# Kernel optimization log

Measured on AMD Instinct MI355X. Metric: run time of the kernel, lower is better.

The kernel has to match this reference:

```python
import jax, jax.numpy as jnp
import numpy as np

PATCH = 16; EMBED = 768; HEADS = 12; DHEAD = 64
DEPTH_PRE = 2; DEPTH_SHORT = 8; PRIOR = 0.2
SCALE = 1.0 / float(DHEAD) ** 0.5
LN_EPS = 1e-5


def _ln(x, g, b):
    m = jnp.mean(x, -1, keepdims=True)
    v = jnp.mean(jnp.square(x - m), -1, keepdims=True)
    return (x - m) * jax.lax.rsqrt(v + LN_EPS) * g + b


def _pos_emb(T, d):
    # pos_seq = T-1 .. 0 (descending), sinusoidal [T, d]
    pos = jnp.arange(T - 1, -1, -1, dtype=jnp.float32)
    inv_freq = 1.0 / (10000.0 ** (jnp.arange(0.0, d, 2.0, dtype=jnp.float32) / d))
    s = pos[:, None] * inv_freq[None, :]
    return jnp.concatenate([jnp.sin(s), jnp.cos(s)], axis=-1)


def _rel_shift(x):
    # Transformer-XL relative shift: pad one zero col, reshape, drop first row
    b, h, q, r = x.shape
    xp = jnp.pad(x, ((0, 0), (0, 0), (0, 0), (1, 0)))
    return xp.reshape(b, h, r + 1, q)[:, :, 1:, :].reshape(b, h, q, r)


def _layer(x, r_emb, rwb, rrb, qkv_w, qkv_b, rn_w, rn_b, o_w, o_b,
           l1g, l1b, f1w, f1b, f2w, f2b, l2g, l2b):
    T, B, D = x.shape
    heads = x @ qkv_w.T + qkv_b
    q, k, v = jnp.split(heads, 3, axis=-1)
    q = q.reshape(T, B, HEADS, DHEAD)
    k = k.reshape(T, B, HEADS, DHEAD)
    v = v.reshape(T, B, HEADS, DHEAD)
    rk = (r_emb @ rn_w.T + rn_b).reshape(T, HEADS, DHEAD)
    AC = jnp.einsum('ibnd,jbnd->bnij', q + rwb, k)
    BD = _rel_shift(jnp.einsum('ibnd,jnd->bnij', q + rrb, rk))
    prob = jax.nn.softmax(SCALE * (AC + BD), axis=-1)  # no attn_mask in this model
    av = jnp.einsum('bnij,jbnd->ibnd', prob, v).reshape(T, B, D)
    x = _ln(x + av @ o_w.T + o_b, l1g, l1b)  # post-lnorm
    h = jax.nn.gelu(x @ f1w.T + f1b, approximate=False)
    return _ln(x + h @ f2w.T + f2b, l2g, l2b)


def setup_inputs() -> dict:
    key = jax.random.key(0)
    ks = jax.random.split(key, 16)
    f = jnp.float32
    D, H, FF, L = EMBED, HEADS, 3072, DEPTH_PRE + DEPTH_SHORT

    def w(k, shape, s=0.02):
        return jax.random.normal(k, shape, dtype=f) * s

    return {
        'x': jax.random.normal(ks[0], (32, 3, 224, 224), dtype=f),
        'patch_w': w(ks[1], (D, 3, PATCH, PATCH)),
        'patch_b': jnp.zeros((D,), f),
        'r_w_bias': jnp.zeros((H, DHEAD), f),
        'r_r_bias': jnp.zeros((H, DHEAD), f),
        'qkv_w': w(ks[2], (L, 3 * D, D)),
        'qkv_b': jnp.zeros((L, 3 * D), f),
        'rnet_w': w(ks[3], (L, D, D)),
        'rnet_b': jnp.zeros((L, D), f),
        'onet_w': w(ks[4], (L, D, D)),
        'onet_b': jnp.zeros((L, D), f),
        'ln1_g': jnp.ones((L, D), f), 'ln1_b': jnp.zeros((L, D), f),
        'ff1_w': w(ks[5], (L, FF, D)),
        'ff1_b': jnp.zeros((L, FF), f),
        'ff2_w': w(ks[6], (L, D, FF)),
        'ff2_b': jnp.zeros((L, D), f),
        'ln2_g': jnp.ones((L, D), f), 'ln2_b': jnp.zeros((L, D), f),
        'null_tok': w(ks[7], (1, 1, D)),
        'down_g': jnp.ones((D,), f), 'down_b': jnp.zeros((D,), f),
        'head_w': w(ks[8], (1000, D)),
        'head_b': jnp.zeros((1000,), f),
    }


def reference(x, patch_w, patch_b, r_w_bias, r_r_bias, qkv_w, qkv_b,
              rnet_w, rnet_b, onet_w, onet_b, ln1_g, ln1_b,
              ff1_w, ff1_b, ff2_w, ff2_b, ln2_g, ln2_b,
              null_tok, down_g, down_b, head_w, head_b):
    B = x.shape[0]
    # patch embed: conv stride=kernel=PATCH, NCHW
    h = jax.lax.conv_general_dilated(
        x, patch_w, (PATCH, PATCH), 'VALID',
        dimension_numbers=('NCHW', 'OIHW', 'NCHW')) + patch_b[None, :, None, None]
    T = h.shape[2] * h.shape[3]  # 196
    h = h.reshape(B, EMBED, T).transpose(2, 0, 1)  # [T, B, D]
    r = _pos_emb(T, EMBED)

    def blk(z, i, rr):
        return _layer(z, rr, r_w_bias, r_r_bias,
                      qkv_w[i], qkv_b[i], rnet_w[i], rnet_b[i],
                      onet_w[i], onet_b[i], ln1_g[i], ln1_b[i],
                      ff1_w[i], ff1_b[i], ff2_w[i], ff2_b[i],
                      ln2_g[i], ln2_b[i])

    for i in range(DEPTH_PRE):
        h = blk(h, i, r)

    # flop_measure boundaries: 1 every interval tokens; downsample = segment mean
    interval = max(1, int(1 / PRIOR))  # 5
    bnd = (jnp.arange(T) % interval == 0).astype(h.dtype)
    seg = (jnp.cumsum(bnd) - bnd).astype(jnp.int32)  # segment id per token
    S = int(np.ceil(T / interval))  # 40 (static)
    onehot = jax.nn.one_hot(seg, S, dtype=h.dtype)  # [T, S]
    pool = onehot / jnp.sum(onehot, axis=0, keepdims=True)
    short = jnp.einsum('tbd,ts->sbd', h, pool)  # [S, B, D]
    short = jnp.concatenate(
        [jnp.broadcast_to(null_tok.reshape(1, 1, EMBED), (1, B, EMBED)), short], axis=0)
    h = _ln(short, down_g, down_b)  # [S+1, B, D]

    r2 = _pos_emb(h.shape[0], EMBED)
    for i in range(DEPTH_PRE, DEPTH_PRE + DEPTH_SHORT):
        h = blk(h, i, r2)

    return h.mean(axis=0) @ head_w.T + head_b  # [B, 1000]
```

## Files before the change

kernel.cpp:

```cpp
#include <hip/hip_runtime.h>
#include <hip/hip_bf16.h>
#include <math.h>
#include <stdint.h>

typedef __bf16 bf16;
typedef __bf16 bf16x8 __attribute__((ext_vector_type(8)));
typedef float  f32x4  __attribute__((ext_vector_type(4)));

#define NB   32
#define ED   768
#define NH   12
#define DHD  64
#define FFD  3072
#define TT1  196
#define TT2  41
#define TPM  208
#define MM1  6272
#define MM2  1408
#define M2R  1312
#define BHN  384
#define LTOT 10
#define SCL  0.125f

__device__ __forceinline__ void gload_lds16(const bf16* g, bf16* l) {
  __builtin_amdgcn_global_load_lds(
      (__attribute__((address_space(1))) void*)(uintptr_t)g,
      (__attribute__((address_space(3))) void*)(uint32_t)(uintptr_t)l,
      16, 0, 0);
}

__device__ __forceinline__ float block_sum(float v, float* red, int tid) {
#pragma unroll
  for (int o = 32; o; o >>= 1) v += __shfl_xor(v, o);
  if ((tid & 63) == 0) red[tid >> 6] = v;
  __syncthreads();
  float t = red[0] + red[1] + red[2] + red[3];
  __syncthreads();
  return t;
}

__device__ __forceinline__ float gelu_f(float v) {
  const float u = v * (0.7978845608f + 0.0356774081f * v * v);
  const float t = 1.0f - 2.0f / (__expf(2.0f * u) + 1.0f);
  return 0.5f * v * (1.0f + t);
}

__device__ __forceinline__ bf16x8 cvt8(const float* __restrict__ s) {
  const f32x4 a = *(const f32x4*)s;
  const f32x4 b = *(const f32x4*)(s + 4);
  bf16x8 o;
#pragma unroll
  for (int j = 0; j < 4; ++j) { o[j] = (bf16)a[j]; o[4 + j] = (bf16)b[j]; }
  return o;
}

__global__ void k_cvt(const float* __restrict__ s, bf16* __restrict__ d, long n8) {
  for (long i = (long)blockIdx.x * 256 + threadIdx.x; i < n8; i += (long)gridDim.x * 256)
    *(bf16x8*)&d[i * 8] = cvt8(&s[i * 8]);
}

__global__ void k_cvt4(const float* __restrict__ a, const float* __restrict__ b,
                       const float* __restrict__ c, const float* __restrict__ d,
                       bf16* __restrict__ oa, bf16* __restrict__ ob,
                       bf16* __restrict__ oc, bf16* __restrict__ od,
                       int na8, int nb8, int nc8, int nd8) {
  const long tot = (long)na8 + nb8 + nc8 + nd8;
  for (long i = (long)blockIdx.x * 256 + threadIdx.x; i < tot; i += (long)gridDim.x * 256) {
    if (i < na8) *(bf16x8*)&oa[i * 8] = cvt8(&a[i * 8]);
    else if (i < (long)na8 + nb8) { const long j = i - na8; *(bf16x8*)&ob[j * 8] = cvt8(&b[j * 8]); }
    else if (i < (long)na8 + nb8 + nc8) { const long j = i - na8 - nb8; *(bf16x8*)&oc[j * 8] = cvt8(&c[j * 8]); }
    else { const long j = i - na8 - nb8 - nc8; *(bf16x8*)&od[j * 8] = cvt8(&d[j * 8]); }
  }
}

__global__ void k_posemb(bf16* __restrict__ out, int T) {
  const int t = blockIdx.x, c = threadIdx.x;
  float v = 0.0f;
  if (t < T) {
    const float pos = (float)(T - 1 - t);
    const int ci = (c < 384) ? c : c - 384;
    const float invf = expf(-(float)ci * (9.210340371976184f / 384.0f));
    const float a = pos * invf;
    v = (c < 384) ? sinf(a) : cosf(a);
  }
  out[(long)t * ED + c] = (bf16)v;
}

__global__ void k_im2col(const float* __restrict__ x, bf16* __restrict__ A0) {
  const long idx = (long)blockIdx.x * 256 + threadIdx.x;
  if (idx >= (long)MM1 * ED) return;
  const int row = (int)(idx / ED), k = (int)(idx % ED);
  const int t = row >> 5, b = row & 31;
  const int c = k >> 8, rem = k & 255, i = rem >> 4, j = rem & 15;
  const int py = t / 14, px = t % 14;
  A0[idx] = (bf16)x[((long)(b * 3 + c) * 224 + (py * 16 + i)) * 224 + px * 16 + j];
}

template <int EPI>
__global__ __launch_bounds__(256) void k_gemm(const bf16* __restrict__ A, const bf16* __restrict__ Bw,
                                              const float* __restrict__ bias,
                                              float* __restrict__ Cf, bf16* __restrict__ Cb,
                                              int M, int N, int K, int LDK) {
  __shared__ __align__(16) bf16 As[3][128 * 32];
  __shared__ __align__(16) bf16 Bs[3][128 * 32];
  const int tid = threadIdx.x;
  const int l = tid & 63, w = tid >> 6;
  const int wr = w >> 1, wc = w & 1;
  const int m0 = blockIdx.y * 128, n0 = blockIdx.x * 128;
  const long koff = (long)blockIdx.z * K;
  const int srow = l >> 2;
  const int scol = ((l & 3) ^ ((l >> 3) & 3)) * 8;
  f32x4 acc[4][4] = {};
  const int nt = K >> 5;

  auto stage = [&](int t, int b) {
    const int kt = t << 5;
#pragma unroll
    for (int p = 0; p < 2; ++p) {
      const int rbase = w * 32 + p * 16;
      gload_lds16(&A[(long)(m0 + rbase + srow) * LDK + koff + kt + scol], &As[b][rbase * 32]);
      gload_lds16(&Bw[(long)(n0 + rbase + srow) * LDK + koff + kt + scol], &Bs[b][rbase * 32]);
    }
  };

  stage(0, 0);
  stage(1, 1);

  int cur = 0;
  for (int t = 0; t < nt; ++t) {
    if (t + 2 < nt) {
      stage(t + 2, cur == 0 ? 2 : cur - 1);
      asm volatile("s_waitcnt vmcnt(8)" ::: "memory");
    } else if (t + 1 < nt) {
      asm volatile("s_waitcnt vmcnt(4)" ::: "memory");
    } else {
      asm volatile("s_waitcnt vmcnt(0)" ::: "memory");
    }
    __builtin_amdgcn_s_barrier();
    {
      bf16x8 af[4], bg[4];
      const int ub = l >> 4;
#pragma unroll
      for (int m = 0; m < 4; ++m) {
        const int row = wr * 64 + m * 16 + (l & 15);
        af[m] = *(const bf16x8*)&As[cur][row * 32 + (ub ^ ((row >> 1) & 3)) * 8];
      }
#pragma unroll
      for (int n = 0; n < 4; ++n) {
        const int row = wc * 64 + n * 16 + (l & 15);
        bg[n] = *(const bf16x8*)&Bs[cur][row * 32 + (ub ^ ((row >> 1) & 3)) * 8];
      }
#pragma unroll
      for (int m = 0; m < 4; ++m)
#pragma unroll
        for (int n = 0; n < 4; ++n)
          acc[m][n] = __builtin_amdgcn_mfma_f32_16x16x32_bf16(af[m], bg[n], acc[m][n], 0, 0, 0);
    }
    asm volatile("s_waitcnt lgkmcnt(0)" ::: "memory");
    __builtin_amdgcn_s_barrier();
    cur = (cur == 2) ? 0 : cur + 1;
  }

  const long pbase = (EPI == 4) ? (long)blockIdx.z * M * N : 0;
#pragma unroll
  for (int m = 0; m < 4; ++m) {
    const int row = m0 + wr * 64 + m * 16 + 4 * (l >> 4);
#pragma unroll
    for (int n = 0; n < 4; ++n) {
      const int col = n0 + wc * 64 + n * 16 + (l & 15);
      const float bv = (EPI == 4) ? 0.0f : bias[col];
#pragma unroll
      for (int r = 0; r < 4; ++r) {
        const float v = acc[m][n][r] + bv;
        const long off = (long)(row + r) * N + col;
        if (EPI == 0) {
          Cf[off] = v;
        } else if (EPI == 1) {
          Cb[off] = (bf16)gelu_f(v);
        } else if (EPI == 2) {
          Cf[off] = v;
          Cb[off] = (bf16)v;
        } else if (EPI == 3) {
          Cb[off] = (bf16)v;
        } else {
          Cf[pbase + off] = v;
        }
      }
    }
  }
}

__global__ __launch_bounds__(256) void k_redk_ln(const float* __restrict__ P, const float* __restrict__ bias,
                                                 const float* __restrict__ g, const float* __restrict__ bb,
                                                 const float* __restrict__ xin,
                                                 float* __restrict__ xo, bf16* __restrict__ xbo,
                                                 int KS, long MN, int Mreal) {
  const int row = blockIdx.x, tid = threadIdx.x;
  const long base = (long)row * ED;
  __shared__ float red[4];
  if (row >= Mreal) {
#pragma unroll
    for (int e = 0; e < 3; ++e) { xo[base + tid + e * 256] = 0.0f; xbo[base + tid + e * 256] = (bf16)0.0f; }
    return;
  }
  float v[3];
#pragma unroll
  for (int e = 0; e < 3; ++e) {
    const int c = tid + e * 256;
    float a = bias[c] + xin[base + c];
    for (int ks = 0; ks < KS; ++ks) a += P[(long)ks * MN + base + c];
    v[e] = a;
  }
  const float mean = block_sum(v[0] + v[1] + v[2], red, tid) * (1.0f / ED);
  float sq = 0.0f;
#pragma unroll
  for (int e = 0; e < 3; ++e) { const float dd = v[e] - mean; sq += dd * dd; }
  const float var = block_sum(sq, red, tid) * (1.0f / ED);
  const float rs = rsqrtf(var + 1e-5f);
#pragma unroll
  for (int e = 0; e < 3; ++e) {
    const int c = tid + e * 256;
    const float o = (v[e] - mean) * rs * g[c] + bb[c];
    xo[base + c] = o;
    xbo[base + c] = (bf16)o;
  }
}

__global__ __launch_bounds__(256) void k_attn_pre(
    const bf16* __restrict__ heads, const float* __restrict__ rwb, const float* __restrict__ rrb,
    const bf16* __restrict__ rkb_l, bf16* __restrict__ avb) {
  const int r0 = blockIdx.x * 64;
  const int bh = blockIdx.y;
  const int b = bh / NH, n = bh % NH;
  const int tid = threadIdx.x;
  const int l = tid & 63, w = tid >> 6;
  __shared__ float Sl[64 * 209];
  __shared__ __align__(16) bf16 probl[64 * 232];
  __shared__ __align__(16) bf16 vTl[64 * 232];
  __shared__ float red4[256];
  __shared__ float rstat[64];

  for (int task = tid; task < 224 * 8; task += 256) {
    const int j = task >> 3, c8 = (task & 7) * 8;
    if (j < TT1) {
      const bf16x8 vv = *(const bf16x8*)&heads[((long)(j * NB + b)) * (3 * ED) + 2 * ED + n * 64 + c8];
#pragma unroll
      for (int e = 0; e < 8; ++e) vTl[(c8 + e) * 232 + j] = vv[e];
    } else {
#pragma unroll
      for (int e = 0; e < 8; ++e) vTl[(c8 + e) * 232 + j] = (bf16)0.0f;
    }
  }

  for (int tt = w; tt < 52; tt += 4) {
    const int ti = tt / 13, tj = tt % 13;
    const int ar = r0 + ti * 16 + (l & 15);
    const int br = tj * 16 + (l & 15);
    f32x4 c = {};
#pragma unroll
    for (int kk = 0; kk < 64; kk += 32) {
      const int col = kk + 8 * (l >> 4);
      bf16x8 qa = {}, kb = {};
      if (ar < TT1) qa = *(const bf16x8*)&heads[((long)(ar * NB + b)) * (3 * ED) + n * 64 + col];
      if (br < TT1) kb = *(const bf16x8*)&heads[((long)(br * NB + b)) * (3 * ED) + ED + n * 64 + col];
      bf16x8 qq;
#pragma unroll
      for (int e = 0; e < 8; ++e) qq[e] = (bf16)((float)qa[e] + rwb[n * 64 + col + e]);
      c = __builtin_amdgcn_mfma_f32_16x16x32_bf16(qq, kb, c, 0, 0, 0);
    }
    const int scol = tj * 16 + (l & 15);
    const int srb = ti * 16 + 4 * (l >> 4);
#pragma unroll
    for (int r = 0; r < 4; ++r) Sl[(srb + r) * 209 + scol] = SCL * c[r];
  }
  __syncthreads();

  for (int tt = w; tt < 65; tt += 4) {
    const int ta = tt / 13, tb = tt % 13;
    const int ar = r0 + ta * 16 + (l & 15);
    const int br = tb * 16 + (l & 15);
    f32x4 c = {};
#pragma unroll
    for (int kk = 0; kk < 64; kk += 32) {
      const int col = kk + 8 * (l >> 4);
      bf16x8 qa = {};
      if (ar < TT1) qa = *(const bf16x8*)&heads[((long)(ar * NB + b)) * (3 * ED) + n * 64 + col];
      const bf16x8 rk = *(const bf16x8*)&rkb_l[((long)n * TPM + br) * 64 + col];
      bf16x8 qq;
#pragma unroll
      for (int e = 0; e < 8; ++e) qq[e] = (bf16)((float)qa[e] + rrb[n * 64 + col + e]);
      c = __builtin_amdgcn_mfma_f32_16x16x32_bf16(qq, rk, c, 0, 0, 0);
    }
    const int bcol = tb * 16 + (l & 15);
    const int ab = r0 + ta * 16 + 4 * (l >> 4);
#pragma unroll
    for (int r = 0; r < 4; ++r) {
      const int a = ab + r;
      if (a < TT1 && bcol < TT1) {
        const int m = a * (TT1 + 1) + bcol + 1;
        if (m >= TT1) {
          const int i = m / TT1 - 1;
          const int j = m - (i + 1) * TT1;
          const int li = i - r0;
          if (li >= 0 && li < 64) Sl[li * 209 + j] += SCL * c[r];
        }
      }
    }
  }
  __syncthreads();

  const int sr = tid & 63, sg = tid >> 6;
  const bool rowok = (r0 + sr) < TT1;
  float pm = -3.0e38f;
  if (rowok) {
    const int j0 = sg * 49;
    for (int j = j0; j < j0 + 49; ++j) pm = fmaxf(pm, Sl[sr * 209 + j]);
  }
  red4[sr * 4 + sg] = pm;
  __syncthreads();
  if (sg == 0)
    rstat[sr] = fmaxf(fmaxf(red4[sr * 4], red4[sr * 4 + 1]), fmaxf(red4[sr * 4 + 2], red4[sr * 4 + 3]));
  __syncthreads();
  const float rm = rstat[sr];
  float ps = 0.0f;
  if (rowok) {
    const int j0 = sg * 49;
    for (int j = j0; j < j0 + 49; ++j) {
      const float e = __expf(Sl[sr * 209 + j] - rm);
      Sl[sr * 209 + j] = e;
      ps += e;
    }
  }
  red4[sr * 4 + sg] = ps;
  __syncthreads();
  if (sg == 0) {
    const float s = red4[sr * 4] + red4[sr * 4 + 1] + red4[sr * 4 + 2] + red4[sr * 4 + 3];
    rstat[sr] = (s > 0.0f) ? 1.0f / s : 0.0f;
  }
  __syncthreads();
  const float inv = rstat[sr];
  for (int j = sg * 56; j < sg * 56 + 56; ++j) {
    const float v = (rowok && j < TT1) ? Sl[sr * 209 + j] * inv : 0.0f;
    probl[sr * 232 + j] = (bf16)v;
  }
  __syncthreads();

  for (int tt = w; tt < 16; tt += 4) {
    const int ti = tt & 3, dj = tt >> 2;
    f32x4 c = {};
#pragma unroll
    for (int kk = 0; kk < 224; kk += 32) {
      const bf16x8 pa = *(const bf16x8*)&probl[(ti * 16 + (l & 15)) * 232 + kk + 8 * (l >> 4)];
      const bf16x8 vb = *(const bf16x8*)&vTl[(dj * 16 + (l & 15)) * 232 + kk + 8 * (l >> 4)];
      c = __builtin_amdgcn_mfma_f32_16x16x32_bf16(pa, vb, c, 0, 0, 0);
    }
    const int d = dj * 16 + (l & 15);
    const int ib = ti * 16 + 4 * (l >> 4);
#pragma unroll
    for (int r = 0; r < 4; ++r) {
      const int gi = r0 + ib + r;
      if (gi < TT1) avb[((long)(gi * NB + b)) * ED + n * 64 + d] = (bf16)c[r];
    }
  }
}

__global__ __launch_bounds__(256) void k_attn_short(
    const bf16* __restrict__ heads, const float* __restrict__ rwb, const float* __restrict__ rrb,
    const bf16* __restrict__ rkb_l, bf16* __restrict__ avb) {
  const int bh = blockIdx.x;
  const int b = bh / NH, n = bh % NH;
  const int tid = threadIdx.x;
  const int l = tid & 63, w = tid >> 6;
  __shared__ float Sl[48 * 49];
  __shared__ __align__(16) bf16 probl[48 * 72];
  __shared__ __align__(16) bf16 vTl[64 * 72];

  for (int task = tid; task < 48 * 8; task += 256) {
    const int j = task >> 3, c8 = (task & 7) * 8;
    if (j < TT2) {
      const bf16x8 vv = *(const bf16x8*)&heads[((long)(j * NB + b)) * (3 * ED) + 2 * ED + n * 64 + c8];
#pragma unroll
      for (int e = 0; e < 8; ++e) vTl[(c8 + e) * 72 + j] = vv[e];
    } else {
#pragma unroll
      for (int e = 0; e < 8; ++e) vTl[(c8 + e) * 72 + j] = (bf16)0.0f;
    }
  }
  for (int idx = tid; idx < 64 * 16; idx += 256)
    vTl[(idx & 63) * 72 + 48 + (idx >> 6)] = (bf16)0.0f;

  for (int tt = w; tt < 9; tt += 4) {
    const int ti = tt / 3, tj = tt % 3;
    const int ar = ti * 16 + (l & 15);
    const int br = tj * 16 + (l & 15);
    f32x4 c = {};
#pragma unroll
    for (int kk = 0; kk < 64; kk += 32) {
      const int col = kk + 8 * (l >> 4);
      bf16x8 qa = {}, kb = {};
      if (ar < 44) qa = *(const bf16x8*)&heads[((long)(ar * NB + b)) * (3 * ED) + n * 64 + col];
      if (br < 44) kb = *(const bf16x8*)&heads[((long)(br * NB + b)) * (3 * ED) + ED + n * 64 + col];
      bf16x8 qq;
#pragma unroll
      for (int e = 0; e < 8; ++e) qq[e] = (bf16)((float)qa[e] + rwb[n * 64 + col + e]);
      c = __builtin_amdgcn_mfma_f32_16x16x32_bf16(qq, kb, c, 0, 0, 0);
    }
    const int scol = tj * 16 + (l & 15);
    const int srb = ti * 16 + 4 * (l >> 4);
#pragma unroll
    for (int r = 0; r < 4; ++r) Sl[(srb + r) * 49 + scol] = SCL * c[r];
  }
  __syncthreads();

  for (int tt = w; tt < 9; tt += 4) {
    const int ti = tt / 3, tj = tt % 3;
    const int ar = ti * 16 + (l & 15);
    const int br = tj * 16 + (l & 15);
    f32x4 c = {};
#pragma unroll
    for (int kk = 0; kk < 64; kk += 32) {
      const int col = kk + 8 * (l >> 4);
      bf16x8 qa = {};
      if (ar < 44) qa = *(const bf16x8*)&heads[((long)(ar * NB + b)) * (3 * ED) + n * 64 + col];
      const bf16x8 rk = *(const bf16x8*)&rkb_l[((long)n * TPM + br) * 64 + col];
      bf16x8 qq;
#pragma unroll
      for (int e = 0; e < 8; ++e) qq[e] = (bf16)((float)qa[e] + rrb[n * 64 + col + e]);
      c = __builtin_amdgcn_mfma_f32_16x16x32_bf16(qq, rk, c, 0, 0, 0);
    }
    const int bcol = tj * 16 + (l & 15);
    const int ab = ti * 16 + 4 * (l >> 4);
#pragma unroll
    for (int r = 0; r < 4; ++r) {
      const int a = ab + r;
      if (a < TT2 && bcol < TT2) {
        const int m = a * (TT2 + 1) + bcol + 1;
        if (m >= TT2) {
          const int i = m / TT2 - 1;
          const int j = m - (i + 1) * TT2;
          Sl[i * 49 + j] += SCL * c[r];
        }
      }
    }
  }
  __syncthreads();

  if (tid < 48) {
    const int i = tid;
    if (i < TT2) {
      float mx = -3.0e38f;
      for (int j = 0; j < TT2; ++j) mx = fmaxf(mx, Sl[i * 49 + j]);
      float sm = 0.0f;
      for (int j = 0; j < TT2; ++j) { const float e = expf(Sl[i * 49 + j] - mx); Sl[i * 49 + j] = e; sm += e; }
      const float inv = 1.0f / sm;
      for (int j = 0; j < TT2; ++j) probl[i * 72 + j] = (bf16)(Sl[i * 49 + j] * inv);
      for (int j = TT2; j < 64; ++j) probl[i * 72 + j] = (bf16)0.0f;
    } else {
      for (int j = 0; j < 64; ++j) probl[i * 72 + j] = (bf16)0.0f;
    }
  }
  __syncthreads();

  for (int tt = w; tt < 12; tt += 4) {
    const int ti = tt % 3, dj = tt / 3;
    f32x4 c = {};
#pragma unroll
    for (int kk = 0; kk < 64; kk += 32) {
      const bf16x8 pa = *(const bf16x8*)&probl[(ti * 16 + (l & 15)) * 72 + kk + 8 * (l >> 4)];
      const bf16x8 vb = *(const bf16x8*)&vTl[(dj * 16 + (l & 15)) * 72 + kk + 8 * (l >> 4)];
      c = __builtin_amdgcn_mfma_f32_16x16x32_bf16(pa, vb, c, 0, 0, 0);
    }
    const int d = dj * 16 + (l & 15);
    const int ib = ti * 16 + 4 * (l >> 4);
#pragma unroll
    for (int r = 0; r < 4; ++r) {
      const int i = ib + r;
      if (i < TT2) avb[((long)(i * NB + b)) * ED + n * 64 + d] = (bf16)c[r];
    }
  }
}

__global__ void k_rkrepack(const float* __restrict__ rkall, bf16* __restrict__ rkb,
                           int T, int Ncols, int l0) {
  const int i = blockIdx.x, z = blockIdx.y, d = threadIdx.x;
  const float v = (i < T) ? rkall[(long)i * Ncols + z * ED + d] : 0.0f;
  const int n = d >> 6, dh = d & 63;
  rkb[(((long)(l0 + z) * NH + n) * TPM + i) * 64 + dh] = (bf16)v;
}

__global__ __launch_bounds__(256) void k_ln(const float* __restrict__ xin, const float* __restrict__ add,
                                            const float* __restrict__ g, const float* __restrict__ bb,
                                            float* __restrict__ xo, bf16* __restrict__ xbo, int Mreal) {
  const int row = blockIdx.x, tid = threadIdx.x;
  const long base = (long)row * ED;
  __shared__ float red[4];
  if (row >= Mreal) {
#pragma unroll
    for (int e = 0; e < 3; ++e) { xo[base + tid + e * 256] = 0.0f; xbo[base + tid + e * 256] = (bf16)0.0f; }
    return;
  }
  float v[3];
#pragma unroll
  for (int e = 0; e < 3; ++e) v[e] = xin[base + tid + e * 256] + add[base + tid + e * 256];
  const float mean = block_sum(v[0] + v[1] + v[2], red, tid) * (1.0f / ED);
  float sq = 0.0f;
#pragma unroll
  for (int e = 0; e < 3; ++e) { const float dd = v[e] - mean; sq += dd * dd; }
  const float var = block_sum(sq, red, tid) * (1.0f / ED);
  const float rs = rsqrtf(var + 1e-5f);
#pragma unroll
  for (int e = 0; e < 3; ++e) {
    const int c = tid + e * 256;
    const float o = (v[e] - mean) * rs * g[c] + bb[c];
    xo[base + c] = o;
    xbo[base + c] = (bf16)o;
  }
}

__global__ __launch_bounds__(256) void k_down(const float* __restrict__ x, const float* __restrict__ nullt,
                                              const float* __restrict__ g, const float* __restrict__ bb,
                                              float* __restrict__ xo, bf16* __restrict__ xbo) {
  const int row = blockIdx.x, tid = threadIdx.x;
  const long base = (long)row * ED;
  __shared__ float red[4];
  if (row >= TT2 * NB) {
#pragma unroll
    for (int e = 0; e < 3; ++e) { xo[base + tid + e * 256] = 0.0f; xbo[base + tid + e * 256] = (bf16)0.0f; }
    return;
  }
  const int s = row >> 5, b = row & 31;
  float v[3];
  if (s == 0) {
#pragma unroll
    for (int e = 0; e < 3; ++e) v[e] = nullt[tid + e * 256];
  } else {
    const int seg = s - 1;
    const int t0 = (seg == 0) ? 0 : (5 * seg - 4);
    const int cnt = (seg == 0) ? 1 : 5;
#pragma unroll
    for (int e = 0; e < 3; ++e) {
      float a = 0.0f;
      for (int tt = 0; tt < cnt; ++tt) a += x[((long)((t0 + tt) * NB + b)) * ED + tid + e * 256];
      v[e] = a / (float)cnt;
    }
  }
  const float mean = block_sum(v[0] + v[1] + v[2], red, tid) * (1.0f / ED);
  float sq = 0.0f;
#pragma unroll
  for (int e = 0; e < 3; ++e) { const float dd = v[e] - mean; sq += dd * dd; }
  const float var = block_sum(sq, red, tid) * (1.0f / ED);
  const float rs = rsqrtf(var + 1e-5f);
#pragma unroll
  for (int e = 0; e < 3; ++e) {
    const int c = tid + e * 256;
    const float o = (v[e] - mean) * rs * g[c] + bb[c];
    xo[base + c] = o;
    xbo[base + c] = (bf16)o;
  }
}

__global__ __launch_bounds__(256) void k_mean(const float* __restrict__ x2, float* __restrict__ xm) {
  const int b = blockIdx.x, tid = threadIdx.x;
#pragma unroll
  for (int e = 0; e < 3; ++e) {
    const int c = tid + e * 256;
    float a = 0.0f;
    for (int s = 0; s < TT2; ++s) a += x2[((long)(s * NB + b)) * ED + c];
    xm[(long)b * ED + c] = a * (1.0f / TT2);
  }
}

__global__ __launch_bounds__(256) void k_head(const float* __restrict__ xm, const float* __restrict__ hw,
                                              const float* __restrict__ hbias, float* __restrict__ out) {
  const int gid = blockIdx.x * 4 + (threadIdx.x >> 6);
  const int l = threadIdx.x & 63;
  if (gid >= NB * 1000) return;
  const int b = gid / 1000, n = gid % 1000;
  const float* xr = xm + (long)b * ED;
  const float* wr = hw + (long)n * ED;
  float a = 0.0f;
#pragma unroll
  for (int e = 0; e < 12; ++e) a += xr[l + 64 * e] * wr[l + 64 * e];
#pragma unroll
  for (int o = 32; o; o >>= 1) a += __shfl_xor(a, o);
  if (l == 0) out[(long)b * 1000 + n] = a + hbias[n];
}

extern "C" void kernel_launch(void* const* d_in, const int* in_sizes, int n_in,
                              void* d_out, int out_size, void* d_ws, size_t ws_size,
                              hipStream_t stream) {
  const float* in_x     = (const float*)d_in[0];
  const float* patch_w  = (const float*)d_in[1];
  const float* patch_b  = (const float*)d_in[2];
  const float* r_w_bias = (const float*)d_in[3];
  const float* r_r_bias = (const float*)d_in[4];
  const float* qkv_w    = (const float*)d_in[5];
  const float* qkv_b    = (const float*)d_in[6];
  const float* rnet_w   = (const float*)d_in[7];
  const float* rnet_b   = (const float*)d_in[8];
  const float* onet_w   = (const float*)d_in[9];
  const float* onet_b   = (const float*)d_in[10];
  const float* ln1_g    = (const float*)d_in[11];
  const float* ln1_b    = (const float*)d_in[12];
  const float* ff1_w    = (const float*)d_in[13];
  const float* ff1_b    = (const float*)d_in[14];
  const float* ff2_w    = (const float*)d_in[15];
  const float* ff2_b    = (const float*)d_in[16];
  const float* ln2_g    = (const float*)d_in[17];
  const float* ln2_b    = (const float*)d_in[18];
  const float* null_tok = (const float*)d_in[19];
  const float* down_g   = (const float*)d_in[20];
  const float* down_b   = (const float*)d_in[21];
  const float* head_w   = (const float*)d_in[22];
  const float* head_b   = (const float*)d_in[23];
  float* out = (float*)d_out;

  char* base = (char*)d_ws;
  size_t off = 0;
  auto take = [&](size_t bytes) -> char* {
    char* r = base + off;
    off += (bytes + 255) & ~(size_t)255;
    return r;
  };

  float* x    = (float*)take((size_t)MM1 * ED * 4);
  bf16*  xb   = (bf16*)take((size_t)MM1 * ED * 2);
  float* x2   = (float*)take((size_t)MM2 * ED * 4);
  bf16*  xb2  = (bf16*)take((size_t)MM2 * ED * 2);
  bf16*  rkb  = (bf16*)take((size_t)LTOT * NH * TPM * 64 * 2);
  bf16*  rbf  = (bf16*)take((size_t)256 * ED * 2);
  bf16*  r2bf = (bf16*)take((size_t)128 * ED * 2);
  float* xm   = (float*)take((size_t)NB * ED * 4);

  char* arenaW = take((size_t)(2304 * 768 + 768 * 768 + 3072 * 768 + 768 * 3072) * 2);
  bf16* wq = (bf16*)arenaW;
  bf16* wo = wq + (size_t)2304 * 768;
  bf16* w1 = wo + (size_t)768 * 768;
  bf16* w2 = w1 + (size_t)3072 * 768;
  bf16* wrnet  = (bf16*)arenaW;
  bf16* wpatch = wrnet + (size_t)LTOT * 768 * 768;

  char* arenaQ = take((size_t)MM1 * ED * 2 + (size_t)4 * MM2 * ED * 4);
  bf16*  A0 = (bf16*)arenaQ;
  float* P  = (float*)arenaQ;

  char* arenaH = take((size_t)MM1 * 3 * ED * 2);
  bf16*  headsb = (bf16*)arenaH;
  float* rkall1 = (float*)arenaH;
  float* rkall2 = (float*)(arenaH + (size_t)256 * 1536 * 4);

  char* arenaS = take((size_t)MM1 * ED * 2 + (size_t)MM1 * ED * 4 + (size_t)MM1 * FFD * 2);
  bf16*  avb  = (bf16*)arenaS;
  float* gout = (float*)(arenaS + (size_t)MM1 * ED * 2);
  bf16*  hb   = (bf16*)(arenaS + (size_t)MM1 * ED * 2 + (size_t)MM1 * ED * 4);

  if (off > ws_size) return;

  k_posemb<<<dim3(256), dim3(768), 0, stream>>>(rbf, TT1);
  k_posemb<<<dim3(128), dim3(768), 0, stream>>>(r2bf, TT2);
  k_cvt<<<dim3(1024), dim3(256), 0, stream>>>(rnet_w, wrnet, (long)LTOT * 768 * 768 / 8);
  k_cvt<<<dim3(288), dim3(256), 0, stream>>>(patch_w, wpatch, (long)768 * 768 / 8);
  k_im2col<<<dim3((MM1 * ED + 255) / 256), dim3(256), 0, stream>>>(in_x, A0);
  k_gemm<2><<<dim3(6, 49, 1), dim3(256), 0, stream>>>(A0, wpatch, patch_b, x, xb, MM1, ED, ED, ED);
  k_gemm<0><<<dim3(12, 2, 1), dim3(256), 0, stream>>>(rbf, wrnet, rnet_b, rkall1, nullptr, 256, 1536, ED, ED);
  k_gemm<0><<<dim3(48, 1, 1), dim3(256), 0, stream>>>(r2bf, wrnet + (size_t)2 * 768 * 768, rnet_b + 2 * 768,
                                                      rkall2, nullptr, 128, 6144, ED, ED);
  k_rkrepack<<<dim3(TPM, 2), dim3(768), 0, stream>>>(rkall1, rkb, TT1, 1536, 0);
  k_rkrepack<<<dim3(48, 8), dim3(768), 0, stream>>>(rkall2, rkb, TT2, 6144, 2);

  for (int l = 0; l < LTOT; ++l) {
    const bool pre = (l < 2);
    const int Mp = pre ? MM1 : MM2;
    const int Mreal = pre ? MM1 : M2R;
    float* xcur = pre ? x : x2;
    bf16* xbcur = pre ? xb : xb2;

    k_cvt4<<<dim3(1024), dim3(256), 0, stream>>>(
        qkv_w + (size_t)l * 2304 * 768, onet_w + (size_t)l * 768 * 768,
        ff1_w + (size_t)l * 3072 * 768, ff2_w + (size_t)l * 768 * 3072,
        wq, wo, w1, w2, 2304 * 768 / 8, 768 * 768 / 8, 3072 * 768 / 8, 768 * 3072 / 8);

    k_gemm<3><<<dim3(18, Mp / 128, 1), dim3(256), 0, stream>>>(xbcur, wq, qkv_b + (size_t)l * 2304,
                                                               nullptr, headsb, Mp, 3 * ED, ED, ED);
    if (pre) {
      k_attn_pre<<<dim3(4, BHN), dim3(256), 0, stream>>>(
          headsb, r_w_bias, r_r_bias, rkb + (size_t)l * NH * TPM * 64, avb);
      k_gemm<0><<<dim3(6, Mp / 128, 1), dim3(256), 0, stream>>>(avb, wo, onet_b + (size_t)l * 768,
                                                                gout, nullptr, Mp, ED, ED, ED);
      k_ln<<<dim3(Mp), dim3(256), 0, stream>>>(xcur, gout, ln1_g + (size_t)l * 768, ln1_b + (size_t)l * 768,
                                               xcur, xbcur, Mreal);
      k_gemm<1><<<dim3(24, Mp / 128, 1), dim3(256), 0, stream>>>(xbcur, w1, ff1_b + (size_t)l * 3072,
                                                                 nullptr, hb, Mp, FFD, ED, ED);
      k_gemm<0><<<dim3(6, Mp / 128, 1), dim3(256), 0, stream>>>(hb, w2, ff2_b + (size_t)l * 768,
                                                                gout, nullptr, Mp, ED, FFD, FFD);
      k_ln<<<dim3(Mp), dim3(256), 0, stream>>>(xcur, gout, ln2_g + (size_t)l * 768, ln2_b + (size_t)l * 768,
                                               xcur, xbcur, Mreal);
    } else {
      k_attn_short<<<dim3(BHN), dim3(256), 0, stream>>>(
          headsb, r_w_bias, r_r_bias, rkb + (size_t)l * NH * TPM * 64, avb);
      k_gemm<4><<<dim3(6, Mp / 128, 2), dim3(256), 0, stream>>>(avb, wo, nullptr,
                                                                P, nullptr, Mp, ED, 384, ED);
      k_redk_ln<<<dim3(Mp), dim3(256), 0, stream>>>(P, onet_b + (size_t)l * 768,
                                                    ln1_g + (size_t)l * 768, ln1_b + (size_t)l * 768,
                                                    xcur, xcur, xbcur, 2, (long)Mp * ED, Mreal);
      k_gemm<1><<<dim3(24, Mp / 128, 1), dim3(256), 0, stream>>>(xbcur, w1, ff1_b + (size_t)l * 3072,
                                                                 nullptr, hb, Mp, FFD, ED, ED);
      k_gemm<4><<<dim3(6, Mp / 128, 4), dim3(256), 0, stream>>>(hb, w2, nullptr,
                                                                P, nullptr, Mp, ED, 768, FFD);
      k_redk_ln<<<dim3(Mp), dim3(256), 0, stream>>>(P, ff2_b + (size_t)l * 768,
                                                    ln2_g + (size_t)l * 768, ln2_b + (size_t)l * 768,
                                                    xcur, xcur, xbcur, 4, (long)Mp * ED, Mreal);
    }

    if (l == 1) {
      k_down<<<dim3(MM2), dim3(256), 0, stream>>>(x, null_tok, down_g, down_b, x2, xb2);
    }
  }

  k_mean<<<dim3(NB), dim3(256), 0, stream>>>(x2, xm);
  k_head<<<dim3(8000), dim3(256), 0, stream>>>(xm, head_w, head_b, out);
}
```

Measured before the change: 1.634 ms.

## Register-reuse Q fragments, prefetch K/R tiles, and XOR-swizzle LDS in attention

In the pre-downsample attention kernel, each wave now keeps its Q+rwb fragment in registers and sweeps all K column tiles, prefetching the next K tile. The BD pass holds all five Q+rrb row-tile fragments in registers per wave and iterates over R tiles with prefetch. The old code reloaded Q and recomputed the bias add for every tile. The prob and transposed-V LDS buffers in both attention kernels use an XOR swizzle on the column index to reduce bank conflicts on the MFMA operand reads. The cost is higher register pressure from the ten held Q fragments, and the swizzle must stay consistent between the writers and the readers.

```diff
diff --git a/kernel.cpp b/kernel.cpp
--- a/kernel.cpp
+++ b/kernel.cpp
@@ -234,6 +234,8 @@
   const int b = bh / NH, n = bh % NH;
   const int tid = threadIdx.x;
   const int l = tid & 63, w = tid >> 6;
+  const int fr = l & 15;
+  const int fc = 8 * (l >> 4);
   __shared__ float Sl[64 * 209];
   __shared__ __align__(16) bf16 probl[64 * 232];
   __shared__ __align__(16) bf16 vTl[64 * 232];
@@ -242,69 +244,104 @@
 
   for (int task = tid; task < 224 * 8; task += 256) {
     const int j = task >> 3, c8 = (task & 7) * 8;
-    if (j < TT1) {
-      const bf16x8 vv = *(const bf16x8*)&heads[((long)(j * NB + b)) * (3 * ED) + 2 * ED + n * 64 + c8];
-#pragma unroll
-      for (int e = 0; e < 8; ++e) vTl[(c8 + e) * 232 + j] = vv[e];
-    } else {
-#pragma unroll
-      for (int e = 0; e < 8; ++e) vTl[(c8 + e) * 232 + j] = (bf16)0.0f;
-    }
-  }
-
-  for (int tt = w; tt < 52; tt += 4) {
-    const int ti = tt / 13, tj = tt % 13;
-    const int ar = r0 + ti * 16 + (l & 15);
-    const int br = tj * 16 + (l & 15);
-    f32x4 c = {};
-#pragma unroll
-    for (int kk = 0; kk < 64; kk += 32) {
-      const int col = kk + 8 * (l >> 4);
-      bf16x8 qa = {}, kb = {};
-      if (ar < TT1) qa = *(const bf16x8*)&heads[((long)(ar * NB + b)) * (3 * ED) + n * 64 + col];
-      if (br < TT1) kb = *(const bf16x8*)&heads[((long)(br * NB + b)) * (3 * ED) + ED + n * 64 + col];
-      bf16x8 qq;
-#pragma unroll
-      for (int e = 0; e < 8; ++e) qq[e] = (bf16)((float)qa[e] + rwb[n * 64 + col + e]);
-      c = __builtin_amdgcn_mfma_f32_16x16x32_bf16(qq, kb, c, 0, 0, 0);
-    }
-    const int scol = tj * 16 + (l & 15);
-    const int srb = ti * 16 + 4 * (l >> 4);
-#pragma unroll
-    for (int r = 0; r < 4; ++r) Sl[(srb + r) * 209 + scol] = SCL * c[r];
-  }
-  __syncthreads();
-
-  for (int tt = w; tt < 65; tt += 4) {
-    const int ta = tt / 13, tb = tt % 13;
-    const int ar = r0 + ta * 16 + (l & 15);
-    const int br = tb * 16 + (l & 15);
-    f32x4 c = {};
-#pragma unroll
-    for (int kk = 0; kk < 64; kk += 32) {
-      const int col = kk + 8 * (l >> 4);
-      bf16x8 qa = {};
-      if (ar < TT1) qa = *(const bf16x8*)&heads[((long)(ar * NB + b)) * (3 * ED) + n * 64 + col];
-      const bf16x8 rk = *(const bf16x8*)&rkb_l[((long)n * TPM + br) * 64 + col];
-      bf16x8 qq;
-#pragma unroll
-      for (int e = 0; e < 8; ++e) qq[e] = (bf16)((float)qa[e] + rrb[n * 64 + col + e]);
-      c = __builtin_amdgcn_mfma_f32_16x16x32_bf16(qq, rk, c, 0, 0, 0);
-    }
-    const int bcol = tb * 16 + (l & 15);
-    const int ab = r0 + ta * 16 + 4 * (l >> 4);
-#pragma unroll
-    for (int r = 0; r < 4; ++r) {
-      const int a = ab + r;
-      if (a < TT1 && bcol < TT1) {
-        const int m = a * (TT1 + 1) + bcol + 1;
-        if (m >= TT1) {
-          const int i = m / TT1 - 1;
-          const int j = m - (i + 1) * TT1;
-          const int li = i - r0;
-          if (li >= 0 && li < 64) Sl[li * 209 + j] += SCL * c[r];
+    bf16x8 vv = {};
+    if (j < TT1) vv = *(const bf16x8*)&heads[((long)(j * NB + b)) * (3 * ED) + 2 * ED + n * 64 + c8];
+#pragma unroll
+    for (int e = 0; e < 8; ++e) {
+      const int d = c8 + e;
+      vTl[d * 232 + (j ^ (((d >> 3) & 3) << 3))] = vv[e];
+    }
+  }
+
+  {
+    const int ti = w;
+    const int ar = r0 + ti * 16 + fr;
+    bf16x8 qa0 = {}, qa1 = {};
+    if (ar < TT1) {
+      const bf16* qp = &heads[((long)(ar * NB + b)) * (3 * ED) + n * 64];
+      qa0 = *(const bf16x8*)(qp + fc);
+      qa1 = *(const bf16x8*)(qp + 32 + fc);
+    }
+    bf16x8 q0, q1;
+#pragma unroll
+    for (int e = 0; e < 8; ++e) {
+      q0[e] = (bf16)((float)qa0[e] + rwb[n * 64 + fc + e]);
+      q1[e] = (bf16)((float)qa1[e] + rwb[n * 64 + 32 + fc + e]);
+    }
+    auto ldk = [&](int tj, bf16x8& k0, bf16x8& k1) {
+      const int br = tj * 16 + fr;
+      k0 = bf16x8{}; k1 = bf16x8{};
+      if (br < TT1) {
+        const bf16* kp = &heads[((long)(br * NB + b)) * (3 * ED) + ED + n * 64];
+        k0 = *(const bf16x8*)(kp + fc);
+        k1 = *(const bf16x8*)(kp + 32 + fc);
+      }
+    };
+    bf16x8 k0, k1, nk0, nk1;
+    ldk(0, k0, k1);
+    for (int tj = 0; tj < 13; ++tj) {
+      if (tj + 1 < 13) ldk(tj + 1, nk0, nk1);
+      f32x4 c = {};
+      c = __builtin_amdgcn_mfma_f32_16x16x32_bf16(q0, k0, c, 0, 0, 0);
+      c = __builtin_amdgcn_mfma_f32_16x16x32_bf16(q1, k1, c, 0, 0, 0);
+      const int scol = tj * 16 + fr;
+      const int srb = ti * 16 + 4 * (l >> 4);
+#pragma unroll
+      for (int r = 0; r < 4; ++r) Sl[(srb + r) * 209 + scol] = SCL * c[r];
+      k0 = nk0; k1 = nk1;
+    }
+  }
+  __syncthreads();
+
+  {
+    bf16x8 qr0[5], qr1[5];
+#pragma unroll
+    for (int ta = 0; ta < 5; ++ta) {
+      const int ar = r0 + ta * 16 + fr;
+      bf16x8 qa0 = {}, qa1 = {};
+      if (ar < TT1) {
+        const bf16* qp = &heads[((long)(ar * NB + b)) * (3 * ED) + n * 64];
+        qa0 = *(const bf16x8*)(qp + fc);
+        qa1 = *(const bf16x8*)(qp + 32 + fc);
+      }
+#pragma unroll
+      for (int e = 0; e < 8; ++e) {
+        qr0[ta][e] = (bf16)((float)qa0[e] + rrb[n * 64 + fc + e]);
+        qr1[ta][e] = (bf16)((float)qa1[e] + rrb[n * 64 + 32 + fc + e]);
+      }
+    }
+    auto ldr = [&](int tb, bf16x8& g0, bf16x8& g1) {
+      const int br = tb * 16 + fr;
+      const bf16* rp = &rkb_l[((long)n * TPM + br) * 64];
+      g0 = *(const bf16x8*)(rp + fc);
+      g1 = *(const bf16x8*)(rp + 32 + fc);
+    };
+    bf16x8 g0, g1, ng0, ng1;
+    if (w < 13) ldr(w, g0, g1);
+    for (int tb = w; tb < 13; tb += 4) {
+      if (tb + 4 < 13) ldr(tb + 4, ng0, ng1);
+#pragma unroll
+      for (int ta = 0; ta < 5; ++ta) {
+        f32x4 c = {};
+        c = __builtin_amdgcn_mfma_f32_16x16x32_bf16(qr0[ta], g0, c, 0, 0, 0);
+        c = __builtin_amdgcn_mfma_f32_16x16x32_bf16(qr1[ta], g1, c, 0, 0, 0);
+        const int bcol = tb * 16 + fr;
+        const int ab = r0 + ta * 16 + 4 * (l >> 4);
+#pragma unroll
+        for (int r = 0; r < 4; ++r) {
+          const int a = ab + r;
+          if (a < TT1 && bcol < TT1) {
+            const int m = a * (TT1 + 1) + bcol + 1;
+            if (m >= TT1) {
+              const int i = m / TT1 - 1;
+              const int j = m - (i + 1) * TT1;
+              const int li = i - r0;
+              if (li >= 0 && li < 64) Sl[li * 209 + j] += SCL * c[r];
+            }
+          }
         }
       }
+      g0 = ng0; g1 = ng1;
     }
   }
   __syncthreads();
@@ -339,22 +376,28 @@
   }
   __syncthreads();
   const float inv = rstat[sr];
+  const int sx = ((sr >> 3) & 3) << 3;
   for (int j = sg * 56; j < sg * 56 + 56; ++j) {
     const float v = (rowok && j < TT1) ? Sl[sr * 209 + j] * inv : 0.0f;
-    probl[sr * 232 + j] = (bf16)v;
+    probl[sr * 232 + (j ^ sx)] = (bf16)v;
   }
   __syncthreads();
 
   for (int tt = w; tt < 16; tt += 4) {
     const int ti = tt & 3, dj = tt >> 2;
+    const int prow = ti * 16 + fr;
+    const int vrow = dj * 16 + fr;
+    const int px = ((prow >> 3) & 3) << 3;
+    const int vx = ((vrow >> 3) & 3) << 3;
     f32x4 c = {};
 #pragma unroll
     for (int kk = 0; kk < 224; kk += 32) {
-      const bf16x8 pa = *(const bf16x8*)&probl[(ti * 16 + (l & 15)) * 232 + kk + 8 * (l >> 4)];
-      const bf16x8 vb = *(const bf16x8*)&vTl[(dj * 16 + (l & 15)) * 232 + kk + 8 * (l >> 4)];
+      const int j0 = kk + fc;
+      const bf16x8 pa = *(const bf16x8*)&probl[prow * 232 + (j0 ^ px)];
+      const bf16x8 vb = *(const bf16x8*)&vTl[vrow * 232 + (j0 ^ vx)];
       c = __builtin_amdgcn_mfma_f32_16x16x32_bf16(pa, vb, c, 0, 0, 0);
     }
-    const int d = dj * 16 + (l & 15);
+    const int d = dj * 16 + fr;
     const int ib = ti * 16 + 4 * (l >> 4);
 #pragma unroll
     for (int r = 0; r < 4; ++r) {
@@ -371,32 +414,30 @@
   const int b = bh / NH, n = bh % NH;
   const int tid = threadIdx.x;
   const int l = tid & 63, w = tid >> 6;
+  const int fr = l & 15, fc = 8 * (l >> 4);
   __shared__ float Sl[48 * 49];
   __shared__ __align__(16) bf16 probl[48 * 72];
   __shared__ __align__(16) bf16 vTl[64 * 72];
 
-  for (int task = tid; task < 48 * 8; task += 256) {
+  for (int task = tid; task < 64 * 8; task += 256) {
     const int j = task >> 3, c8 = (task & 7) * 8;
-    if (j < TT2) {
-      const bf16x8 vv = *(const bf16x8*)&heads[((long)(j * NB + b)) * (3 * ED) + 2 * ED + n * 64 + c8];
-#pragma unroll
-      for (int e = 0; e < 8; ++e) vTl[(c8 + e) * 72 + j] = vv[e];
-    } else {
-#pragma unroll
-      for (int e = 0; e < 8; ++e) vTl[(c8 + e) * 72 + j] = (bf16)0.0f;
-    }
-  }
-  for (int idx = tid; idx < 64 * 16; idx += 256)
-    vTl[(idx & 63) * 72 + 48 + (idx >> 6)] = (bf16)0.0f;
+    bf16x8 vv = {};
+    if (j < TT2) vv = *(const bf16x8*)&heads[((long)(j * NB + b)) * (3 * ED) + 2 * ED + n * 64 + c8];
+#pragma unroll
+    for (int e = 0; e < 8; ++e) {
+      const int d = c8 + e;
+      vTl[d * 72 + (j ^ (((d >> 3) & 3) << 3))] = vv[e];
+    }
+  }
 
   for (int tt = w; tt < 9; tt += 4) {
     const int ti = tt / 3, tj = tt % 3;
-    const int ar = ti * 16 + (l & 15);
-    const int br = tj * 16 + (l & 15);
+    const int ar = ti * 16 + fr;
+    const int br = tj * 16 + fr;
     f32x4 c = {};
 #pragma unroll
     for (int kk = 0; kk < 64; kk += 32) {
-      const int col = kk + 8 * (l >> 4);
+      const int col = kk + fc;
       bf16x8 qa = {}, kb = {};
       if (ar < 44) qa = *(const bf16x8*)&heads[((long)(ar * NB + b)) * (3 * ED) + n * 64 + col];
       if (br < 44) kb = *(const bf16x8*)&heads[((long)(br * NB + b)) * (3 * ED) + ED + n * 64 + col];
@@ -405,7 +446,7 @@
       for (int e = 0; e < 8; ++e) qq[e] = (bf16)((float)qa[e] + rwb[n * 64 + col + e]);
       c = __builtin_amdgcn_mfma_f32_16x16x32_bf16(qq, kb, c, 0, 0, 0);
     }
-    const int scol = tj * 16 + (l & 15);
+    const int scol = tj * 16 + fr;
     const int srb = ti * 16 + 4 * (l >> 4);
 #pragma unroll
     for (int r = 0; r < 4; ++r) Sl[(srb + r) * 49 + scol] = SCL * c[r];
@@ -414,12 +455,12 @@
 
   for (int tt = w; tt < 9; tt += 4) {
     const int ti = tt / 3, tj = tt % 3;
-    const int ar = ti * 16 + (l & 15);
-    const int br = tj * 16 + (l & 15);
+    const int ar = ti * 16 + fr;
+    const int br = tj * 16 + fr;
     f32x4 c = {};
 #pragma unroll
     for (int kk = 0; kk < 64; kk += 32) {
-      const int col = kk + 8 * (l >> 4);
+      const int col = kk + fc;
       bf16x8 qa = {};
       if (ar < 44) qa = *(const bf16x8*)&heads[((long)(ar * NB + b)) * (3 * ED) + n * 64 + col];
       const bf16x8 rk = *(const bf16x8*)&rkb_l[((long)n * TPM + br) * 64 + col];
@@ -428,7 +469,7 @@
       for (int e = 0; e < 8; ++e) qq[e] = (bf16)((float)qa[e] + rrb[n * 64 + col + e]);
       c = __builtin_amdgcn_mfma_f32_16x16x32_bf16(qq, rk, c, 0, 0, 0);
     }
-    const int bcol = tj * 16 + (l & 15);
+    const int bcol = tj * 16 + fr;
     const int ab = ti * 16 + 4 * (l >> 4);
 #pragma unroll
     for (int r = 0; r < 4; ++r) {
@@ -447,30 +488,36 @@
 
   if (tid < 48) {
     const int i = tid;
+    const int ix = ((i >> 3) & 3) << 3;
     if (i < TT2) {
       float mx = -3.0e38f;
       for (int j = 0; j < TT2; ++j) mx = fmaxf(mx, Sl[i * 49 + j]);
       float sm = 0.0f;
       for (int j = 0; j < TT2; ++j) { const float e = expf(Sl[i * 49 + j] - mx); Sl[i * 49 + j] = e; sm += e; }
       const float inv = 1.0f / sm;
-      for (int j = 0; j < TT2; ++j) probl[i * 72 + j] = (bf16)(Sl[i * 49 + j] * inv);
-      for (int j = TT2; j < 64; ++j) probl[i * 72 + j] = (bf16)0.0f;
+      for (int j = 0; j < TT2; ++j) probl[i * 72 + (j ^ ix)] = (bf16)(Sl[i * 49 + j] * inv);
+      for (int j = TT2; j < 64; ++j) probl[i * 72 + (j ^ ix)] = (bf16)0.0f;
     } else {
-      for (int j = 0; j < 64; ++j) probl[i * 72 + j] = (bf16)0.0f;
+      for (int j = 0; j < 64; ++j) probl[i * 72 + (j ^ ix)] = (bf16)0.0f;
     }
   }
   __syncthreads();
 
   for (int tt = w; tt < 12; tt += 4) {
     const int ti = tt % 3, dj = tt / 3;
+    const int prow = ti * 16 + fr;
+    const int vrow = dj * 16 + fr;
+    const int px = ((prow >> 3) & 3) << 3;
+    const int vx = ((vrow >> 3) & 3) << 3;
     f32x4 c = {};
 #pragma unroll
     for (int kk = 0; kk < 64; kk += 32) {
-      const bf16x8 pa = *(const bf16x8*)&probl[(ti * 16 + (l & 15)) * 72 + kk + 8 * (l >> 4)];
-      const bf16x8 vb = *(const bf16x8*)&vTl[(dj * 16 + (l & 15)) * 72 + kk + 8 * (l >> 4)];
+      const int j0 = kk + fc;
+      const bf16x8 pa = *(const bf16x8*)&probl[prow * 72 + (j0 ^ px)];
+      const bf16x8 vb = *(const bf16x8*)&vTl[vrow * 72 + (j0 ^ vx)];
       c = __builtin_amdgcn_mfma_f32_16x16x32_bf16(pa, vb, c, 0, 0, 0);
     }
-    const int d = dj * 16 + (l & 15);
+    const int d = dj * 16 + fr;
     const int ib = ti * 16 + 4 * (l >> 4);
 #pragma unroll
     for (int r = 0; r < 4; ++r) {
```

New measurement: 1.542 ms. 1.06x faster.
